# Performance work log

Measured on AMD Instinct MI355X. Metric: run time of the kernel, lower is better.

Reference implementation:

```python
import jax, jax.numpy as jnp
import numpy as np

N_STATE = 1024
N_HEAD = 16
D_K = N_STATE // N_HEAD  # 64


def setup_inputs() -> dict:
    key = jax.random.key(0)
    ks = jax.random.split(key, 12)
    B, S = 2, 2048
    s = 1.0 / np.sqrt(N_STATE)
    inp = {
        "q": jax.random.normal(ks[0], (B, S, N_STATE), jnp.float32),
        "k": jax.random.normal(ks[1], (B, S, N_STATE), jnp.float32),
        "v": jax.random.normal(ks[2], (B, S, N_STATE), jnp.float32),
        # Linear weights in torch layout [out_features, in_features]
        "Wq": jax.random.normal(ks[3], (N_STATE, N_STATE), jnp.float32) * s,
        "bq": jax.random.normal(ks[4], (N_STATE,), jnp.float32) * s,
        "Wk": jax.random.normal(ks[5], (N_STATE, N_STATE), jnp.float32) * s,
        "bk": jax.random.normal(ks[6], (N_STATE,), jnp.float32) * s,
        "Wv": jax.random.normal(ks[7], (N_STATE, N_STATE), jnp.float32) * s,
        "bv": jax.random.normal(ks[8], (N_STATE,), jnp.float32) * s,
        "Wo": jax.random.normal(ks[9], (N_STATE, N_STATE), jnp.float32) * s,
        "bo": jax.random.normal(ks[10], (N_STATE,), jnp.float32) * s,
    }
    return inp


def reference(q, k, v, Wq, bq, Wk, bk, Wv, bv, Wo, bo):
    B = q.shape[0]
    # projections (torch Linear: x @ W.T + b), split heads -> [B, H, S, d]
    def proj(x, W, b):
        y = jnp.einsum('bsi,oi->bso', x, W) + b
        return y.reshape(B, -1, N_HEAD, D_K).transpose(0, 2, 1, 3)
    qh = proj(q, Wq, bq)
    kh = proj(k, Wk, bk)
    vh = proj(v, Wv, bv)
    # scaled dot-product attention, full [B,H,Sq,Sk] scores as in original
    scores = jnp.einsum('bhqd,bhkd->bhqk', qh, kh) / np.sqrt(D_K).astype(np.float32)
    attn = jax.nn.softmax(scores, axis=-1)
    out = jnp.einsum('bhqk,bhkd->bhqd', attn, vh)
    out = out.transpose(0, 2, 1, 3).reshape(B, -1, N_HEAD * D_K)
    return jnp.einsum('bsi,oi->bso', out, Wo) + bo
```

## Files before the change

### kernel.cpp

```cpp
#include <hip/hip_runtime.h>
#include <stdint.h>

typedef __attribute__((ext_vector_type(8))) short short8;
typedef __attribute__((ext_vector_type(4))) float f32x4;
typedef __attribute__((ext_vector_type(4))) uint32_t u32x4;

#if __has_builtin(__builtin_amdgcn_exp2f)
#define EXP2(x) __builtin_amdgcn_exp2f(x)
#else
#define EXP2(x) exp2f(x)
#endif

__device__ __forceinline__ short f2bf(float f){
  uint32_t u = __builtin_bit_cast(uint32_t, f);
  return (short)((u + 0x8000u) >> 16);
}
__device__ __forceinline__ uint32_t pk2(float lo, float hi){
  uint32_t a = __builtin_bit_cast(uint32_t, lo) + 0x8000u;
  uint32_t b = __builtin_bit_cast(uint32_t, hi) + 0x8000u;
#if __has_builtin(__builtin_amdgcn_perm)
  return __builtin_amdgcn_perm(b, a, 0x07060302u);
#else
  return (b & 0xFFFF0000u) | (a >> 16);
#endif
}
__device__ __forceinline__ void gload16(const void* g, void* l){
  __builtin_amdgcn_global_load_lds((const __attribute__((address_space(1))) void*)g,
                                   (__attribute__((address_space(3))) void*)l, 16, 0, 0);
}

__global__ __launch_bounds__(512) void cvt_all(
    const float* __restrict__ q, const float* __restrict__ k, const float* __restrict__ v,
    const float* __restrict__ wq, const float* __restrict__ wk, const float* __restrict__ wv,
    const float* __restrict__ wo, short* __restrict__ dst){
  const size_t SQ = 4096ull*1024ull, NW = 1024ull*1024ull;
  size_t e = (size_t)(blockIdx.x*512u + threadIdx.x)*8ull;
  const float* src; size_t rel;
  if (e < 3*SQ){ size_t which = e / SQ; src = which==0?q:(which==1?k:v); rel = e - which*SQ; }
  else { size_t e2 = e - 3*SQ; size_t which = e2 / NW;
         src = which==0?wq:(which==1?wk:(which==2?wv:wo)); rel = e2 - which*NW; }
  float4 a = *(const float4*)(src + rel);
  float4 b = *(const float4*)(src + rel + 4);
  u32x4 r = { pk2(a.x,a.y), pk2(a.z,a.w), pk2(b.x,b.y), pk2(b.z,b.w) };
  *(u32x4*)(dst + e) = r;
}

template<int MODE, int NWAVE>
__device__ __forceinline__ void gemm_body(const short* __restrict__ A, const short* __restrict__ Bw,
    const float* __restrict__ bias, void* __restrict__ Cout, float scale, int m0, int n0){
  const int K = 1024;
  const int NT  = NWAVE*64;
  const int SW  = 1024/NT;
  const int RPS = NT/8;
  const int NI  = (NWAVE==4) ? 4 : 2;
  const int WCOL = NI*16;
  __shared__ short Al[128*64];
  __shared__ short Bl[128*64];
  int tid = threadIdx.x;
  int w = tid >> 6, lane = tid & 63, lr = lane & 15, lg = lane >> 4;
  int wr = (NWAVE==4) ? (w >> 1) : (w >> 2);
  int wc = (NWAVE==4) ? (w & 1)  : (w & 3);
  f32x4 acc[4][NI] = {};
  int row0 = tid >> 3;
  int qc0  = (tid & 7) ^ (row0 & 7);
  const short* Ag = A  + (size_t)(m0 + row0)*K + qc0*8;
  const short* Bg = Bw + (size_t)(n0 + row0)*K + qc0*8;
  char* Alb = (char*)Al + tid*16;
  char* Blb = (char*)Bl + tid*16;
  int ra[4], rb[NI];
#pragma unroll
  for (int mi=0; mi<4; ++mi) ra[mi] = wr*64 + mi*16 + lr;
#pragma unroll
  for (int ni=0; ni<NI; ++ni) rb[ni] = wc*WCOL + ni*16 + lr;
  for (int k0 = 0; k0 < K; k0 += 64){
#pragma unroll
    for (int s=0; s<SW; ++s) gload16(Ag + k0 + (size_t)(s*RPS)*K, Alb + s*NT*16);
#pragma unroll
    for (int s=0; s<SW; ++s) gload16(Bg + k0 + (size_t)(s*RPS)*K, Blb + s*NT*16);
    __syncthreads();
#pragma unroll
    for (int kk=0; kk<2; ++kk){
      short8 av[4], bv[NI];
#pragma unroll
      for (int mi=0; mi<4; ++mi)
        av[mi] = *(const short8*)((char*)Al + ra[mi]*128 + (((kk*4 + lg) ^ (ra[mi] & 7)) << 4));
#pragma unroll
      for (int ni=0; ni<NI; ++ni)
        bv[ni] = *(const short8*)((char*)Bl + rb[ni]*128 + (((kk*4 + lg) ^ (rb[ni] & 7)) << 4));
#pragma unroll
      for (int mi=0; mi<4; ++mi)
#pragma unroll
        for (int ni=0; ni<NI; ++ni){
          if (MODE == 2)
            acc[mi][ni] = __builtin_amdgcn_mfma_f32_16x16x32_bf16(bv[ni], av[mi], acc[mi][ni], 0, 0, 0);
          else
            acc[mi][ni] = __builtin_amdgcn_mfma_f32_16x16x32_bf16(av[mi], bv[ni], acc[mi][ni], 0, 0, 0);
        }
    }
    __syncthreads();
  }
#pragma unroll
  for (int ni=0; ni<NI; ++ni){
#pragma unroll
    for (int mi=0; mi<4; ++mi){
      if (MODE == 2){
        int srow = m0 + wr*64 + mi*16 + lr;
        int b = srow >> 11, s = srow & 2047;
#pragma unroll
        for (int i2=0; i2<4; ++i2){
          int dcol = n0 + wc*WCOL + ni*16 + lg*4 + i2;
          int h = dcol >> 6, d = dcol & 63;
          float val = acc[mi][ni][i2] + bias[dcol];
          ((short*)Cout)[(((size_t)(b*16 + h))*64 + d)*2048 + s] = f2bf(val);
        }
      } else {
        int col = n0 + wc*WCOL + ni*16 + lr;
        float bb = bias[col];
#pragma unroll
        for (int i2=0; i2<4; ++i2){
          int row = m0 + wr*64 + mi*16 + lg*4 + i2;
          float val = (acc[mi][ni][i2] + bb) * scale;
          if (MODE == 0){
            int b = row >> 11, s = row & 2047, h = col >> 6, d = col & 63;
            ((short*)Cout)[(((size_t)(b*16 + h))*2048 + s)*64 + d] = f2bf(val);
          } else {
            ((float*)Cout)[(size_t)row*1024 + col] = val;
          }
        }
      }
    }
  }
}

__global__ __launch_bounds__(256) void gemm_qkv(
    const short* __restrict__ qb, const short* __restrict__ kb, const short* __restrict__ vb,
    const short* __restrict__ Wqb, const short* __restrict__ Wkb, const short* __restrict__ Wvb,
    const float* __restrict__ bq, const float* __restrict__ bk, const float* __restrict__ bv,
    short* __restrict__ Qh, short* __restrict__ Kh, short* __restrict__ VhT, float qscale){
  int f = blockIdx.y*gridDim.x + blockIdx.x;
  int L = (f & 7)*96 + (f >> 3);
  int z = L >> 8, r = L & 255;
  int m0 = (r >> 3)*128, n0 = (r & 7)*128;
  const short* A  = z==0 ? qb  : (z==1 ? kb  : vb);
  const short* Bw = z==0 ? Wqb : (z==1 ? Wkb : Wvb);
  const float* bi = z==0 ? bq  : (z==1 ? bk  : bv);
  short* C        = z==0 ? Qh  : (z==1 ? Kh  : VhT);
  if (z == 2) gemm_body<2,4>(A, Bw, bi, (void*)C, 1.0f, m0, n0);
  else        gemm_body<0,4>(A, Bw, bi, (void*)C, z==0 ? qscale : 1.0f, m0, n0);
}

__global__ __launch_bounds__(512) void gemm_out(const short* __restrict__ A, const short* __restrict__ Bw,
    const float* __restrict__ bias, float* __restrict__ Cout){
  int f = blockIdx.y*gridDim.x + blockIdx.x;
  int L = (f & 7)*32 + (f >> 3);
  int m0 = (L >> 3)*128, n0 = (L & 7)*128;
  gemm_body<1,8>(A, Bw, bias, (void*)Cout, 1.0f, m0, n0);
}

__global__ __launch_bounds__(512) void attn_fwd(const short* __restrict__ Qh, const short* __restrict__ Kh,
    const short* __restrict__ VhT, short* __restrict__ AO){
  const int S = 2048;
  int i = blockIdx.y*gridDim.x + blockIdx.x;
  int L = (i & 7)*64 + (i >> 3);
  int bh = L >> 4, qt = L & 15;
  __shared__ short Kl[4][4096];
  __shared__ short Vl[4][4096];
  int tid = threadIdx.x, w = tid >> 6, lane = tid & 63, lr = lane & 15, lg = lane >> 4;
  const short* Qb = Qh  + (size_t)bh*S*64;
  const short* Kb = Kh  + (size_t)bh*S*64;
  const short* Vb = VhT + (size_t)bh*64*2048;
  int q0 = qt*128 + w*16;
  short8 aq[2];
#pragma unroll
  for (int h=0; h<2; ++h)
    aq[h] = *(const short8*)&Qb[(size_t)(q0 + lr)*64 + h*32 + lg*8];
  f32x4 o[4] = {};
  f32x4 o1 = {};
  short8 ones;
#pragma unroll
  for (int j=0; j<8; ++j) ones[j] = (short)0x3F80;
  int koff = tid*16;
  int kr = tid >> 3, kc = tid & 7;
  int ksw = (kr & 3) | (((kr >> 3) & 1) << 2);
  int ksrc = kr*64 + ((kc ^ ksw) << 3);
  int vsrc = kr*2048 + ((kc ^ (kr & 7)) << 3);
  int Rbase = 8*(lr >> 2) + (lr & 3);
  int sR = (lr & 3) | (((lr >> 2) & 1) << 2);
  int slot0 = (lg ^ sR) << 3, slot1 = ((lg + 4) ^ sR) << 3;
  int vx = lr & 7;
#pragma unroll
  for (int t=0; t<4; ++t){
    gload16(Kb + (size_t)t*4096 + ksrc, (char*)&Kl[t][0] + koff);
    gload16(Vb + vsrc + t*64,           (char*)&Vl[t][0] + koff);
  }
  asm volatile("s_waitcnt vmcnt(4)" ::: "memory");
  __builtin_amdgcn_sched_barrier(0);
  __builtin_amdgcn_s_barrier();

  for (int p = 0; p < 16; ++p){
    short8 pa[2][2];
    __builtin_amdgcn_s_setprio(1);
#pragma unroll
    for (int u = 0; u < 2; ++u){
      const short* Kbuf = &Kl[(2*p + u) & 3][0];
      uint32_t Wp[2][2][2];
#pragma unroll
      for (int nf=0; nf<4; ++nf){
        int R = Rbase + (nf & 1)*4 + (nf >> 1)*32;
        short8 ak0 = *(const short8*)&Kbuf[R*64 + slot0];
        short8 ak1 = *(const short8*)&Kbuf[R*64 + slot1];
        f32x4 z = {};
        z = __builtin_amdgcn_mfma_f32_16x16x32_bf16(ak0, aq[0], z, 0, 0, 0);
        z = __builtin_amdgcn_mfma_f32_16x16x32_bf16(ak1, aq[1], z, 0, 0, 0);
        float p0 = EXP2(z[0]), p1 = EXP2(z[1]);
        float p2 = EXP2(z[2]), p3 = EXP2(z[3]);
        Wp[nf >> 1][nf & 1][0] = pk2(p0, p1);
        Wp[nf >> 1][nf & 1][1] = pk2(p2, p3);
      }
#pragma unroll
      for (int c=0; c<2; ++c){
        union { uint32_t u4[4]; short8 s; } tt;
        tt.u4[0] = Wp[c][0][0]; tt.u4[1] = Wp[c][0][1];
        tt.u4[2] = Wp[c][1][0]; tt.u4[3] = Wp[c][1][1];
        pa[u][c] = tt.s;
      }
    }
#pragma unroll
    for (int u = 0; u < 2; ++u){
      const short* Vbuf = &Vl[(2*p + u) & 3][0];
#pragma unroll
      for (int df=0; df<4; ++df){
        int rowv = (df*16 + lr)*64;
        short8 vb0 = *(const short8*)&Vbuf[rowv + ((lg ^ vx) << 3)];
        short8 vb1 = *(const short8*)&Vbuf[rowv + (((4 + lg) ^ vx) << 3)];
        o[df] = __builtin_amdgcn_mfma_f32_16x16x32_bf16(pa[u][0], vb0, o[df], 0, 0, 0);
        o[df] = __builtin_amdgcn_mfma_f32_16x16x32_bf16(pa[u][1], vb1, o[df], 0, 0, 0);
      }
      o1 = __builtin_amdgcn_mfma_f32_16x16x32_bf16(pa[u][0], ones, o1, 0, 0, 0);
      o1 = __builtin_amdgcn_mfma_f32_16x16x32_bf16(pa[u][1], ones, o1, 0, 0, 0);
    }
    __builtin_amdgcn_s_setprio(0);
    if (p < 15){
      asm volatile("s_waitcnt vmcnt(0)" ::: "memory");
      __builtin_amdgcn_sched_barrier(0);
      __builtin_amdgcn_s_barrier();
      if (p < 14){
#pragma unroll
        for (int u = 0; u < 2; ++u){
          int t = 2*p + 4 + u, nb = t & 3;
          gload16(Kb + (size_t)t*4096 + ksrc, (char*)&Kl[nb][0] + koff);
          gload16(Vb + vsrc + t*64,           (char*)&Vl[nb][0] + koff);
        }
      }
    }
  }
  int b = bh >> 4, hh = bh & 15;
  float rinv[4];
#pragma unroll
  for (int i2=0; i2<4; ++i2) rinv[i2] = 1.0f / o1[i2];
#pragma unroll
  for (int df=0; df<4; ++df)
#pragma unroll
    for (int i2=0; i2<4; ++i2){
      int row = q0 + lg*4 + i2;
      int col = df*16 + lr;
      AO[((size_t)(b*2048 + row))*1024 + hh*64 + col] = f2bf(o[df][i2] * rinv[i2]);
    }
}

extern "C" void kernel_launch(void* const* d_in, const int* in_sizes, int n_in,
                              void* d_out, int out_size, void* d_ws, size_t ws_size,
                              hipStream_t stream){
  const float* q  = (const float*)d_in[0];
  const float* k  = (const float*)d_in[1];
  const float* v  = (const float*)d_in[2];
  const float* Wq = (const float*)d_in[3];
  const float* bq = (const float*)d_in[4];
  const float* Wk = (const float*)d_in[5];
  const float* bk = (const float*)d_in[6];
  const float* Wv = (const float*)d_in[7];
  const float* bv = (const float*)d_in[8];
  const float* Wo = (const float*)d_in[9];
  const float* bo = (const float*)d_in[10];

  const size_t SQ = 4096ull*1024ull, NW = 1024ull*1024ull;
  short* ws  = (short*)d_ws;
  short* qb  = ws;
  short* kb  = ws + SQ;
  short* vb  = ws + 2*SQ;
  short* Wqb = ws + 3*SQ;
  short* Wkb = Wqb + NW;
  short* Wvb = Wkb + NW;
  short* Wob = Wvb + NW;
  short* Qh  = Wob + NW;
  short* Kh  = Qh + SQ;
  short* VhT = Kh + SQ;
  short* AO  = qb;

  const float Csc = 0.18033688011112042f;

  cvt_all<<<4096, 512, 0, stream>>>(q, k, v, Wq, Wk, Wv, Wo, ws);
  gemm_qkv<<<dim3(16, 48), 256, 0, stream>>>(qb, kb, vb, Wqb, Wkb, Wvb, bq, bk, bv, Qh, Kh, VhT, Csc);
  attn_fwd<<<dim3(16, 32), 512, 0, stream>>>(Qh, Kh, VhT, AO);
  gemm_out<<<dim3(16, 16), 512, 0, stream>>>(AO, Wob, bo, (float*)d_out);
}
```

Measured before the change: 116.8 us.

## Split attention over key halves with 32-row query tiles and add a merge kernel

Each attention block now handles 256 queries (32 per wave, two MFMA row groups sharing each K/V LDS fragment) over half of the key range. It writes unnormalized bf16 partial outputs and row sums that a new merge kernel adds and normalizes into the head-interleaved layout. This doubles K/V reuse per LDS load while keeping the grid size. The cost is an extra launch, extra global traffic for the partials, and bf16 rounding of the partials before the merge. Separately, the QKV GEMM now runs with 512 threads (8 waves) instead of 256.

```diff
diff --git a/kernel.cpp b/kernel.cpp
--- a/kernel.cpp
+++ b/kernel.cpp
@@ -14,6 +14,9 @@
 __device__ __forceinline__ short f2bf(float f){
   uint32_t u = __builtin_bit_cast(uint32_t, f);
   return (short)((u + 0x8000u) >> 16);
+}
+__device__ __forceinline__ float bf2f(short s){
+  return __builtin_bit_cast(float, (uint32_t)(uint16_t)s << 16);
 }
 __device__ __forceinline__ uint32_t pk2(float lo, float hi){
   uint32_t a = __builtin_bit_cast(uint32_t, lo) + 0x8000u;
@@ -132,7 +135,7 @@
   }
 }
 
-__global__ __launch_bounds__(256) void gemm_qkv(
+__global__ __launch_bounds__(512) void gemm_qkv(
     const short* __restrict__ qb, const short* __restrict__ kb, const short* __restrict__ vb,
     const short* __restrict__ Wqb, const short* __restrict__ Wkb, const short* __restrict__ Wvb,
     const float* __restrict__ bq, const float* __restrict__ bk, const float* __restrict__ bv,
@@ -145,8 +148,8 @@
   const short* Bw = z==0 ? Wqb : (z==1 ? Wkb : Wvb);
   const float* bi = z==0 ? bq  : (z==1 ? bk  : bv);
   short* C        = z==0 ? Qh  : (z==1 ? Kh  : VhT);
-  if (z == 2) gemm_body<2,4>(A, Bw, bi, (void*)C, 1.0f, m0, n0);
-  else        gemm_body<0,4>(A, Bw, bi, (void*)C, z==0 ? qscale : 1.0f, m0, n0);
+  if (z == 2) gemm_body<2,8>(A, Bw, bi, (void*)C, 1.0f, m0, n0);
+  else        gemm_body<0,8>(A, Bw, bi, (void*)C, z==0 ? qscale : 1.0f, m0, n0);
 }
 
 __global__ __launch_bounds__(512) void gemm_out(const short* __restrict__ A, const short* __restrict__ Bw,
@@ -157,25 +160,30 @@
   gemm_body<1,8>(A, Bw, bias, (void*)Cout, 1.0f, m0, n0);
 }
 
-__global__ __launch_bounds__(512) void attn_fwd(const short* __restrict__ Qh, const short* __restrict__ Kh,
-    const short* __restrict__ VhT, short* __restrict__ AO){
+__global__ __launch_bounds__(512, 4) void attn_fwd(const short* __restrict__ Qh, const short* __restrict__ Kh,
+    const short* __restrict__ VhT, short* __restrict__ Op0, short* __restrict__ Op1,
+    float* __restrict__ Ls){
   const int S = 2048;
   int i = blockIdx.y*gridDim.x + blockIdx.x;
   int L = (i & 7)*64 + (i >> 3);
-  int bh = L >> 4, qt = L & 15;
+  int bh = L >> 4, r4 = L & 15;
+  int qt = r4 >> 1, kh = r4 & 1;
   __shared__ short Kl[4][4096];
   __shared__ short Vl[4][4096];
   int tid = threadIdx.x, w = tid >> 6, lane = tid & 63, lr = lane & 15, lg = lane >> 4;
   const short* Qb = Qh  + (size_t)bh*S*64;
-  const short* Kb = Kh  + (size_t)bh*S*64;
-  const short* Vb = VhT + (size_t)bh*64*2048;
-  int q0 = qt*128 + w*16;
-  short8 aq[2];
-#pragma unroll
-  for (int h=0; h<2; ++h)
-    aq[h] = *(const short8*)&Qb[(size_t)(q0 + lr)*64 + h*32 + lg*8];
-  f32x4 o[4] = {};
-  f32x4 o1 = {};
+  const short* Kb = Kh  + (size_t)bh*S*64 + (size_t)kh*16*4096;
+  const short* Vb = VhT + (size_t)bh*64*2048 + (size_t)kh*16*64;
+  short* Op = kh ? Op1 : Op0;
+  int q0 = qt*256 + w*32;
+  short8 aq[2][2];
+#pragma unroll
+  for (int m=0; m<2; ++m)
+#pragma unroll
+    for (int h=0; h<2; ++h)
+      aq[m][h] = *(const short8*)&Qb[(size_t)(q0 + m*16 + lr)*64 + h*32 + lg*8];
+  f32x4 o[2][4] = {};
+  f32x4 o1[2] = {};
   short8 ones;
 #pragma unroll
   for (int j=0; j<8; ++j) ones[j] = (short)0x3F80;
@@ -197,54 +205,65 @@
   __builtin_amdgcn_sched_barrier(0);
   __builtin_amdgcn_s_barrier();
 
-  for (int p = 0; p < 16; ++p){
-    short8 pa[2][2];
+  for (int p = 0; p < 8; ++p){
     __builtin_amdgcn_s_setprio(1);
 #pragma unroll
     for (int u = 0; u < 2; ++u){
-      const short* Kbuf = &Kl[(2*p + u) & 3][0];
-      uint32_t Wp[2][2][2];
-#pragma unroll
-      for (int nf=0; nf<4; ++nf){
-        int R = Rbase + (nf & 1)*4 + (nf >> 1)*32;
-        short8 ak0 = *(const short8*)&Kbuf[R*64 + slot0];
-        short8 ak1 = *(const short8*)&Kbuf[R*64 + slot1];
-        f32x4 z = {};
-        z = __builtin_amdgcn_mfma_f32_16x16x32_bf16(ak0, aq[0], z, 0, 0, 0);
-        z = __builtin_amdgcn_mfma_f32_16x16x32_bf16(ak1, aq[1], z, 0, 0, 0);
-        float p0 = EXP2(z[0]), p1 = EXP2(z[1]);
-        float p2 = EXP2(z[2]), p3 = EXP2(z[3]);
-        Wp[nf >> 1][nf & 1][0] = pk2(p0, p1);
-        Wp[nf >> 1][nf & 1][1] = pk2(p2, p3);
-      }
-#pragma unroll
-      for (int c=0; c<2; ++c){
-        union { uint32_t u4[4]; short8 s; } tt;
-        tt.u4[0] = Wp[c][0][0]; tt.u4[1] = Wp[c][0][1];
-        tt.u4[2] = Wp[c][1][0]; tt.u4[3] = Wp[c][1][1];
-        pa[u][c] = tt.s;
-      }
-    }
-#pragma unroll
-    for (int u = 0; u < 2; ++u){
-      const short* Vbuf = &Vl[(2*p + u) & 3][0];
+      int buf = (2*p + u) & 3;
+      const short* Kbuf = &Kl[buf][0];
+      short8 pa[2][2];
+      {
+        uint32_t Wp[2][2][2][2];
+#pragma unroll
+        for (int nf=0; nf<4; ++nf){
+          int R = Rbase + (nf & 1)*4 + (nf >> 1)*32;
+          short8 ak0 = *(const short8*)&Kbuf[R*64 + slot0];
+          short8 ak1 = *(const short8*)&Kbuf[R*64 + slot1];
+#pragma unroll
+          for (int m=0; m<2; ++m){
+            f32x4 z = {};
+            z = __builtin_amdgcn_mfma_f32_16x16x32_bf16(ak0, aq[m][0], z, 0, 0, 0);
+            z = __builtin_amdgcn_mfma_f32_16x16x32_bf16(ak1, aq[m][1], z, 0, 0, 0);
+            float p0 = EXP2(z[0]), p1 = EXP2(z[1]);
+            float p2 = EXP2(z[2]), p3 = EXP2(z[3]);
+            Wp[m][nf >> 1][nf & 1][0] = pk2(p0, p1);
+            Wp[m][nf >> 1][nf & 1][1] = pk2(p2, p3);
+          }
+        }
+#pragma unroll
+        for (int m=0; m<2; ++m)
+#pragma unroll
+          for (int c=0; c<2; ++c){
+            union { uint32_t u4[4]; short8 s; } tt;
+            tt.u4[0] = Wp[m][c][0][0]; tt.u4[1] = Wp[m][c][0][1];
+            tt.u4[2] = Wp[m][c][1][0]; tt.u4[3] = Wp[m][c][1][1];
+            pa[m][c] = tt.s;
+          }
+      }
+      const short* Vbuf = &Vl[buf][0];
 #pragma unroll
       for (int df=0; df<4; ++df){
         int rowv = (df*16 + lr)*64;
         short8 vb0 = *(const short8*)&Vbuf[rowv + ((lg ^ vx) << 3)];
         short8 vb1 = *(const short8*)&Vbuf[rowv + (((4 + lg) ^ vx) << 3)];
-        o[df] = __builtin_amdgcn_mfma_f32_16x16x32_bf16(pa[u][0], vb0, o[df], 0, 0, 0);
-        o[df] = __builtin_amdgcn_mfma_f32_16x16x32_bf16(pa[u][1], vb1, o[df], 0, 0, 0);
-      }
-      o1 = __builtin_amdgcn_mfma_f32_16x16x32_bf16(pa[u][0], ones, o1, 0, 0, 0);
-      o1 = __builtin_amdgcn_mfma_f32_16x16x32_bf16(pa[u][1], ones, o1, 0, 0, 0);
+#pragma unroll
+        for (int m=0; m<2; ++m){
+          o[m][df] = __builtin_amdgcn_mfma_f32_16x16x32_bf16(pa[m][0], vb0, o[m][df], 0, 0, 0);
+          o[m][df] = __builtin_amdgcn_mfma_f32_16x16x32_bf16(pa[m][1], vb1, o[m][df], 0, 0, 0);
+        }
+      }
+#pragma unroll
+      for (int m=0; m<2; ++m){
+        o1[m] = __builtin_amdgcn_mfma_f32_16x16x32_bf16(pa[m][0], ones, o1[m], 0, 0, 0);
+        o1[m] = __builtin_amdgcn_mfma_f32_16x16x32_bf16(pa[m][1], ones, o1[m], 0, 0, 0);
+      }
     }
     __builtin_amdgcn_s_setprio(0);
-    if (p < 15){
+    if (p < 7){
       asm volatile("s_waitcnt vmcnt(0)" ::: "memory");
       __builtin_amdgcn_sched_barrier(0);
       __builtin_amdgcn_s_barrier();
-      if (p < 14){
+      if (p < 6){
 #pragma unroll
         for (int u = 0; u < 2; ++u){
           int t = 2*p + 4 + u, nb = t & 3;
@@ -254,18 +273,39 @@
       }
     }
   }
-  int b = bh >> 4, hh = bh & 15;
-  float rinv[4];
-#pragma unroll
-  for (int i2=0; i2<4; ++i2) rinv[i2] = 1.0f / o1[i2];
-#pragma unroll
-  for (int df=0; df<4; ++df)
-#pragma unroll
-    for (int i2=0; i2<4; ++i2){
-      int row = q0 + lg*4 + i2;
-      int col = df*16 + lr;
-      AO[((size_t)(b*2048 + row))*1024 + hh*64 + col] = f2bf(o[df][i2] * rinv[i2]);
-    }
+#pragma unroll
+  for (int m=0; m<2; ++m){
+#pragma unroll
+    for (int df=0; df<4; ++df)
+#pragma unroll
+      for (int i2=0; i2<4; ++i2){
+        int row = q0 + m*16 + lg*4 + i2;
+        Op[((size_t)(bh*2048 + row))*64 + df*16 + lr] = f2bf(o[m][df][i2]);
+      }
+    if (lr == 0){
+#pragma unroll
+      for (int i2=0; i2<4; ++i2){
+        int row = q0 + m*16 + lg*4 + i2;
+        Ls[kh*65536 + bh*2048 + row] = o1[m][i2];
+      }
+    }
+  }
+}
+
+__global__ __launch_bounds__(256) void attn_merge(const short* __restrict__ Op0, const short* __restrict__ Op1,
+    const float* __restrict__ Ls, short* __restrict__ AO){
+  size_t e = (size_t)(blockIdx.x*256u + threadIdx.x)*8ull;
+  int d = (int)(e & 63);
+  size_t rowg = e >> 6;
+  float rinv = 1.0f / (Ls[rowg] + Ls[65536 + rowg]);
+  short8 a = *(const short8*)&Op0[e];
+  short8 b8 = *(const short8*)&Op1[e];
+  int bh = (int)(rowg >> 11), qq = (int)(rowg & 2047);
+  int b = bh >> 4, h = bh & 15;
+  short8 r;
+#pragma unroll
+  for (int j=0; j<8; ++j) r[j] = f2bf((bf2f(a[j]) + bf2f(b8[j])) * rinv);
+  *(short8*)&AO[((size_t)(b*2048 + qq))*1024 + h*64 + d] = r;
 }
 
 extern "C" void kernel_launch(void* const* d_in, const int* in_sizes, int n_in,
@@ -296,11 +336,15 @@
   short* Kh  = Qh + SQ;
   short* VhT = Kh + SQ;
   short* AO  = qb;
+  short* Op0 = kb;
+  short* Op1 = vb;
+  float* Ls  = (float*)Wqb;
 
   const float Csc = 0.18033688011112042f;
 
   cvt_all<<<4096, 512, 0, stream>>>(q, k, v, Wq, Wk, Wv, Wo, ws);
-  gemm_qkv<<<dim3(16, 48), 256, 0, stream>>>(qb, kb, vb, Wqb, Wkb, Wvb, bq, bk, bv, Qh, Kh, VhT, Csc);
-  attn_fwd<<<dim3(16, 32), 512, 0, stream>>>(Qh, Kh, VhT, AO);
+  gemm_qkv<<<dim3(16, 48), 512, 0, stream>>>(qb, kb, vb, Wqb, Wkb, Wvb, bq, bk, bv, Qh, Kh, VhT, Csc);
+  attn_fwd<<<dim3(16, 32), 512, 0, stream>>>(Qh, Kh, VhT, Op0, Op1, Ls);
+  attn_merge<<<2048, 256, 0, stream>>>(Op0, Op1, Ls, AO);
   gemm_out<<<dim3(16, 16), 512, 0, stream>>>(AO, Wob, bo, (float*)d_out);
 }
```

Result: no change. 117.1 us (+0.2%).
